# Optimization experiments

Measured on AMD Instinct MI355X. Metric: run time of the kernel, lower is better.

The kernel has to match this reference:

```python
import jax, jax.numpy as jnp
import numpy as np

N_NODES = 1_000_000   # total (cell x bin) pseudo nodes
FEAT_DIM = 128        # feature_dim
EMBED_DIM = 128       # embed_dim
BATCH = 8192          # nodes per forward batch
K = 10                # num_sample neighbors per node


def setup_inputs() -> dict:
    key = jax.random.key(0)
    k0, k1, k2, k3, k4 = jax.random.split(key, 5)
    emb = jax.random.normal(k0, (N_NODES, FEAT_DIM), dtype=jnp.float32)
    nodes = jax.random.randint(k1, (BATCH,), 0, N_NODES, dtype=jnp.int32)
    neigh_ids = jax.random.randint(k2, (BATCH, K), 0, N_NODES, dtype=jnp.int32)
    # strictly positive raw weights (contact counts); normalized per-row in forward
    neigh_w = jax.random.uniform(k3, (BATCH, K), dtype=jnp.float32, minval=1e-3, maxval=1.0)
    # nn.Linear(input_size * feat_dim, embed_dim), input_size = 2 (self + neighbors, gcn=False)
    W = jax.random.normal(k4, (2 * FEAT_DIM, EMBED_DIM), dtype=jnp.float32) / np.sqrt(2 * FEAT_DIM)
    b = jnp.zeros((EMBED_DIM,), dtype=jnp.float32)
    return {"emb": emb, "neigh_w": neigh_w, "W": W, "b": b,
            "nodes": nodes, "neigh_ids": neigh_ids}


def reference(emb, neigh_w, W, b, nodes, neigh_ids):
    # per-row weight normalization: w /= np.sum(w)  (weighted mean, replaces the COO spmm)
    w = neigh_w / jnp.sum(neigh_w, axis=1, keepdims=True)          # [B, K]
    neigh_feats = jnp.einsum('bk,bkd->bd', w, emb[neigh_ids])       # gather + weighted mean -> [B, D]
    self_feats = emb[nodes]                                         # [B, D]
    # gcn=False: concat self and aggregated neighbor features, then Linear + swish
    h = jnp.concatenate([self_feats, neigh_feats], axis=-1) @ W + b # [B, E]
    return h * jax.nn.sigmoid(h)                                    # swish activation
```

## Files before the change

kernel.cpp:

```cpp
#include <hip/hip_runtime.h>


#define B_NODES 8192
#define K_NEIGH 10
#define FDIM 128
#define EDIM 128
#define NPB 16
#define THREADS 256

typedef __attribute__((ext_vector_type(8))) short short8v;
typedef __attribute__((ext_vector_type(4))) float float4v;

__device__ __forceinline__ int swz(int byte) {
    return byte ^ (((byte >> 9) & 7) << 4);
}

__device__ __forceinline__ short f2bf(float f) {
    unsigned u = __builtin_bit_cast(unsigned, f);
    u += 0x7FFFu + ((u >> 16) & 1u);
    return (short)(u >> 16);
}

__global__ __launch_bounds__(THREADS, 2) void sage_fused(
    const float* __restrict__ emb,
    const float* __restrict__ neigh_w,
    const float* __restrict__ Wm,
    const float* __restrict__ bias,
    const int*   __restrict__ nodes,
    const int*   __restrict__ neigh_ids,
    float* __restrict__ out)
{
    __shared__ __align__(16) short x_lds[NPB * 2 * FDIM];
    char* xb = (char*)x_lds;

    const int tid = threadIdx.x;
    const int nb0 = blockIdx.x * NPB;

    {
        const int hw  = tid >> 5;
        const int l32 = tid & 31;
        const int d0  = l32 * 4;

        const int nA = hw * 2, nB = nA + 1;
        const int gA = nb0 + nA, gB = nb0 + nB;

        const int sidA = nodes[gA];
        const int sidB = nodes[gB];
        int idsA[K_NEIGH], idsB[K_NEIGH];
        float wA[K_NEIGH], wB[K_NEIGH];
#pragma unroll
        for (int k = 0; k < K_NEIGH; ++k) idsA[k] = neigh_ids[gA * K_NEIGH + k];
#pragma unroll
        for (int k = 0; k < K_NEIGH; ++k) idsB[k] = neigh_ids[gB * K_NEIGH + k];
        float wsA = 0.f, wsB = 0.f;
#pragma unroll
        for (int k = 0; k < K_NEIGH; ++k) { wA[k] = neigh_w[gA * K_NEIGH + k]; wsA += wA[k]; }
#pragma unroll
        for (int k = 0; k < K_NEIGH; ++k) { wB[k] = neigh_w[gB * K_NEIGH + k]; wsB += wB[k]; }
        const float invA = 1.f / wsA, invB = 1.f / wsB;

        {
            const float4 sv = *reinterpret_cast<const float4*>(&emb[(size_t)sidA * FDIM + d0]);
            float4 a = make_float4(0.f, 0.f, 0.f, 0.f);
#pragma unroll
            for (int k = 0; k < K_NEIGH; ++k) {
                const float4 v = *reinterpret_cast<const float4*>(&emb[(size_t)idsA[k] * FDIM + d0]);
                a.x = fmaf(wA[k], v.x, a.x); a.y = fmaf(wA[k], v.y, a.y);
                a.z = fmaf(wA[k], v.z, a.z); a.w = fmaf(wA[k], v.w, a.w);
            }
            ushort4 s4, g4;
            s4.x = (unsigned short)f2bf(sv.x); s4.y = (unsigned short)f2bf(sv.y);
            s4.z = (unsigned short)f2bf(sv.z); s4.w = (unsigned short)f2bf(sv.w);
            g4.x = (unsigned short)f2bf(a.x * invA); g4.y = (unsigned short)f2bf(a.y * invA);
            g4.z = (unsigned short)f2bf(a.z * invA); g4.w = (unsigned short)f2bf(a.w * invA);
            *reinterpret_cast<ushort4*>(xb + swz(nA * 512 + l32 * 8))       = s4;
            *reinterpret_cast<ushort4*>(xb + swz(nA * 512 + 256 + l32 * 8)) = g4;
        }
        {
            const float4 sv = *reinterpret_cast<const float4*>(&emb[(size_t)sidB * FDIM + d0]);
            float4 a = make_float4(0.f, 0.f, 0.f, 0.f);
#pragma unroll
            for (int k = 0; k < K_NEIGH; ++k) {
                const float4 v = *reinterpret_cast<const float4*>(&emb[(size_t)idsB[k] * FDIM + d0]);
                a.x = fmaf(wB[k], v.x, a.x); a.y = fmaf(wB[k], v.y, a.y);
                a.z = fmaf(wB[k], v.z, a.z); a.w = fmaf(wB[k], v.w, a.w);
            }
            ushort4 s4, g4;
            s4.x = (unsigned short)f2bf(sv.x); s4.y = (unsigned short)f2bf(sv.y);
            s4.z = (unsigned short)f2bf(sv.z); s4.w = (unsigned short)f2bf(sv.w);
            g4.x = (unsigned short)f2bf(a.x * invB); g4.y = (unsigned short)f2bf(a.y * invB);
            g4.z = (unsigned short)f2bf(a.z * invB); g4.w = (unsigned short)f2bf(a.w * invB);
            *reinterpret_cast<ushort4*>(xb + swz(nB * 512 + l32 * 8))       = s4;
            *reinterpret_cast<ushort4*>(xb + swz(nB * 512 + 256 + l32 * 8)) = g4;
        }
    }
    __syncthreads();

    {
        const int l    = tid & 63;
        const int wave = tid >> 6;
        const int lg   = l >> 4;
        const int li   = l & 15;

        float4v acc0 = {0.f, 0.f, 0.f, 0.f};
        float4v acc1 = {0.f, 0.f, 0.f, 0.f};
        const int e0 = wave * 32;

#pragma unroll
        for (int kblk = 0; kblk < 8; ++kblk) {
            const short8v a = *reinterpret_cast<const short8v*>(
                xb + swz(li * 512 + kblk * 64 + lg * 16));

            const int kb = kblk * 32 + lg * 8;
            short8v b0, b1;
#pragma unroll
            for (int j = 0; j < 8; ++j) {
                b0[j] = f2bf(Wm[(size_t)(kb + j) * EDIM + e0 + li]);
                b1[j] = f2bf(Wm[(size_t)(kb + j) * EDIM + e0 + 16 + li]);
            }
            acc0 = __builtin_amdgcn_mfma_f32_16x16x32_bf16(a, b0, acc0, 0, 0, 0);
            acc1 = __builtin_amdgcn_mfma_f32_16x16x32_bf16(a, b1, acc1, 0, 0, 0);
        }

        const float bv0 = bias[e0 + li];
        const float bv1 = bias[e0 + 16 + li];
#pragma unroll
        for (int r = 0; r < 4; ++r) {
            const int row = nb0 + lg * 4 + r;
            float v0 = acc0[r] + bv0;
            float v1 = acc1[r] + bv1;
            out[(size_t)row * EDIM + e0 + li]      = v0 / (1.f + __expf(-v0));
            out[(size_t)row * EDIM + e0 + 16 + li] = v1 / (1.f + __expf(-v1));
        }
    }
}

extern "C" void kernel_launch(void* const* d_in, const int* in_sizes, int n_in,
                              void* d_out, int out_size, void* d_ws, size_t ws_size,
                              hipStream_t stream) {
    const float* emb       = (const float*)d_in[0];
    const float* neigh_w   = (const float*)d_in[1];
    const float* Wm        = (const float*)d_in[2];
    const float* bias      = (const float*)d_in[3];
    const int*   nodes     = (const int*)d_in[4];
    const int*   neigh_ids = (const int*)d_in[5];
    float* out = (float*)d_out;

    sage_fused<<<dim3(B_NODES / NPB), dim3(THREADS), 0, stream>>>(
        emb, neigh_w, Wm, bias, nodes, neigh_ids, out);
}
```

Baseline: 16.40 us.

## Halve nodes per block and gather with full-wave float2 lanes per node

Cuts nodes per block from 16 to 8, doubling the grid to 1024 blocks, and raises the launch-bounds occupancy hint to 4. Each wave now gathers two nodes, with 64 lanes each loading float2 slices instead of 32 lanes loading float4. The neighbor id and weight loads are vectorized as int2/float2. The upper half of the LDS tile is zero-filled so the 16-row MFMA still runs, and only the 8 valid rows are written. The goal is more memory-level parallelism for the random embedding gathers, at the cost of wasting half of the MFMA work and reloading W per block twice as often overall.

```diff
diff --git a/kernel.cpp b/kernel.cpp
--- a/kernel.cpp
+++ b/kernel.cpp
@@ -5,7 +5,7 @@
 #define K_NEIGH 10
 #define FDIM 128
 #define EDIM 128
-#define NPB 16
+#define NPB 8
 #define THREADS 256
 
 typedef __attribute__((ext_vector_type(8))) short short8v;
@@ -21,7 +21,7 @@
     return (short)(u >> 16);
 }
 
-__global__ __launch_bounds__(THREADS, 2) void sage_fused(
+__global__ __launch_bounds__(THREADS, 4) void sage_fused(
     const float* __restrict__ emb,
     const float* __restrict__ neigh_w,
     const float* __restrict__ Wm,
@@ -30,81 +30,78 @@
     const int*   __restrict__ neigh_ids,
     float* __restrict__ out)
 {
-    __shared__ __align__(16) short x_lds[NPB * 2 * FDIM];
+    __shared__ __align__(16) short x_lds[16 * 2 * FDIM];
     char* xb = (char*)x_lds;
 
     const int tid = threadIdx.x;
     const int nb0 = blockIdx.x * NPB;
+    const int wv  = tid >> 6;
+    const int l   = tid & 63;
+
+    *reinterpret_cast<float4*>(xb + 4096 + tid * 16) = make_float4(0.f, 0.f, 0.f, 0.f);
 
     {
-        const int hw  = tid >> 5;
-        const int l32 = tid & 31;
-        const int d0  = l32 * 4;
+        const int d0 = l * 2;
+        const int nlA = wv * 2, nlB = nlA + 1;
+        const int gA = nb0 + nlA, gB = nb0 + nlB;
 
-        const int nA = hw * 2, nB = nA + 1;
-        const int gA = nb0 + nA, gB = nb0 + nB;
-
+        const int2*   ipA = reinterpret_cast<const int2*>(neigh_ids + (size_t)gA * K_NEIGH);
+        const int2*   ipB = reinterpret_cast<const int2*>(neigh_ids + (size_t)gB * K_NEIGH);
+        const float2* wpA = reinterpret_cast<const float2*>(neigh_w  + (size_t)gA * K_NEIGH);
+        const float2* wpB = reinterpret_cast<const float2*>(neigh_w  + (size_t)gB * K_NEIGH);
+        int2 idA[5], idB[5];
+        float2 wA[5], wB[5];
+#pragma unroll
+        for (int k = 0; k < 5; ++k) idA[k] = ipA[k];
+#pragma unroll
+        for (int k = 0; k < 5; ++k) idB[k] = ipB[k];
+#pragma unroll
+        for (int k = 0; k < 5; ++k) wA[k] = wpA[k];
+#pragma unroll
+        for (int k = 0; k < 5; ++k) wB[k] = wpB[k];
         const int sidA = nodes[gA];
         const int sidB = nodes[gB];
-        int idsA[K_NEIGH], idsB[K_NEIGH];
-        float wA[K_NEIGH], wB[K_NEIGH];
-#pragma unroll
-        for (int k = 0; k < K_NEIGH; ++k) idsA[k] = neigh_ids[gA * K_NEIGH + k];
-#pragma unroll
-        for (int k = 0; k < K_NEIGH; ++k) idsB[k] = neigh_ids[gB * K_NEIGH + k];
+
         float wsA = 0.f, wsB = 0.f;
 #pragma unroll
-        for (int k = 0; k < K_NEIGH; ++k) { wA[k] = neigh_w[gA * K_NEIGH + k]; wsA += wA[k]; }
-#pragma unroll
-        for (int k = 0; k < K_NEIGH; ++k) { wB[k] = neigh_w[gB * K_NEIGH + k]; wsB += wB[k]; }
+        for (int k = 0; k < 5; ++k) { wsA += wA[k].x + wA[k].y; wsB += wB[k].x + wB[k].y; }
         const float invA = 1.f / wsA, invB = 1.f / wsB;
 
-        {
-            const float4 sv = *reinterpret_cast<const float4*>(&emb[(size_t)sidA * FDIM + d0]);
-            float4 a = make_float4(0.f, 0.f, 0.f, 0.f);
+        const float2 svA = *reinterpret_cast<const float2*>(&emb[(size_t)sidA * FDIM + d0]);
+        const float2 svB = *reinterpret_cast<const float2*>(&emb[(size_t)sidB * FDIM + d0]);
+
+        float axA = 0.f, ayA = 0.f, axB = 0.f, ayB = 0.f;
 #pragma unroll
-            for (int k = 0; k < K_NEIGH; ++k) {
-                const float4 v = *reinterpret_cast<const float4*>(&emb[(size_t)idsA[k] * FDIM + d0]);
-                a.x = fmaf(wA[k], v.x, a.x); a.y = fmaf(wA[k], v.y, a.y);
-                a.z = fmaf(wA[k], v.z, a.z); a.w = fmaf(wA[k], v.w, a.w);
-            }
-            ushort4 s4, g4;
-            s4.x = (unsigned short)f2bf(sv.x); s4.y = (unsigned short)f2bf(sv.y);
-            s4.z = (unsigned short)f2bf(sv.z); s4.w = (unsigned short)f2bf(sv.w);
-            g4.x = (unsigned short)f2bf(a.x * invA); g4.y = (unsigned short)f2bf(a.y * invA);
-            g4.z = (unsigned short)f2bf(a.z * invA); g4.w = (unsigned short)f2bf(a.w * invA);
-            *reinterpret_cast<ushort4*>(xb + swz(nA * 512 + l32 * 8))       = s4;
-            *reinterpret_cast<ushort4*>(xb + swz(nA * 512 + 256 + l32 * 8)) = g4;
+        for (int k = 0; k < 5; ++k) {
+            const float2 vxA = *reinterpret_cast<const float2*>(&emb[(size_t)idA[k].x * FDIM + d0]);
+            const float2 vyA = *reinterpret_cast<const float2*>(&emb[(size_t)idA[k].y * FDIM + d0]);
+            const float2 vxB = *reinterpret_cast<const float2*>(&emb[(size_t)idB[k].x * FDIM + d0]);
+            const float2 vyB = *reinterpret_cast<const float2*>(&emb[(size_t)idB[k].y * FDIM + d0]);
+            axA = fmaf(wA[k].x, vxA.x, axA); ayA = fmaf(wA[k].x, vxA.y, ayA);
+            axA = fmaf(wA[k].y, vyA.x, axA); ayA = fmaf(wA[k].y, vyA.y, ayA);
+            axB = fmaf(wB[k].x, vxB.x, axB); ayB = fmaf(wB[k].x, vxB.y, ayB);
+            axB = fmaf(wB[k].y, vyB.x, axB); ayB = fmaf(wB[k].y, vyB.y, ayB);
         }
-        {
-            const float4 sv = *reinterpret_cast<const float4*>(&emb[(size_t)sidB * FDIM + d0]);
-            float4 a = make_float4(0.f, 0.f, 0.f, 0.f);
-#pragma unroll
-            for (int k = 0; k < K_NEIGH; ++k) {
-                const float4 v = *reinterpret_cast<const float4*>(&emb[(size_t)idsB[k] * FDIM + d0]);
-                a.x = fmaf(wB[k], v.x, a.x); a.y = fmaf(wB[k], v.y, a.y);
-                a.z = fmaf(wB[k], v.z, a.z); a.w = fmaf(wB[k], v.w, a.w);
-            }
-            ushort4 s4, g4;
-            s4.x = (unsigned short)f2bf(sv.x); s4.y = (unsigned short)f2bf(sv.y);
-            s4.z = (unsigned short)f2bf(sv.z); s4.w = (unsigned short)f2bf(sv.w);
-            g4.x = (unsigned short)f2bf(a.x * invB); g4.y = (unsigned short)f2bf(a.y * invB);
-            g4.z = (unsigned short)f2bf(a.z * invB); g4.w = (unsigned short)f2bf(a.w * invB);
-            *reinterpret_cast<ushort4*>(xb + swz(nB * 512 + l32 * 8))       = s4;
-            *reinterpret_cast<ushort4*>(xb + swz(nB * 512 + 256 + l32 * 8)) = g4;
-        }
+
+        ushort2 t;
+        t.x = (unsigned short)f2bf(svA.x); t.y = (unsigned short)f2bf(svA.y);
+        *reinterpret_cast<ushort2*>(xb + swz(nlA * 512 + l * 4)) = t;
+        t.x = (unsigned short)f2bf(axA * invA); t.y = (unsigned short)f2bf(ayA * invA);
+        *reinterpret_cast<ushort2*>(xb + swz(nlA * 512 + 256 + l * 4)) = t;
+        t.x = (unsigned short)f2bf(svB.x); t.y = (unsigned short)f2bf(svB.y);
+        *reinterpret_cast<ushort2*>(xb + swz(nlB * 512 + l * 4)) = t;
+        t.x = (unsigned short)f2bf(axB * invB); t.y = (unsigned short)f2bf(ayB * invB);
+        *reinterpret_cast<ushort2*>(xb + swz(nlB * 512 + 256 + l * 4)) = t;
     }
     __syncthreads();
 
     {
-        const int l    = tid & 63;
-        const int wave = tid >> 6;
-        const int lg   = l >> 4;
-        const int li   = l & 15;
+        const int lg = l >> 4;
+        const int li = l & 15;
+        const int e0 = wv * 32;
 
         float4v acc0 = {0.f, 0.f, 0.f, 0.f};
         float4v acc1 = {0.f, 0.f, 0.f, 0.f};
-        const int e0 = wave * 32;
 
 #pragma unroll
         for (int kblk = 0; kblk < 8; ++kblk) {
@@ -122,15 +119,17 @@
             acc1 = __builtin_amdgcn_mfma_f32_16x16x32_bf16(a, b1, acc1, 0, 0, 0);
         }
 
-        const float bv0 = bias[e0 + li];
-        const float bv1 = bias[e0 + 16 + li];
+        if (lg < 2) {
+            const float bv0 = bias[e0 + li];
+            const float bv1 = bias[e0 + 16 + li];
 #pragma unroll
-        for (int r = 0; r < 4; ++r) {
-            const int row = nb0 + lg * 4 + r;
-            float v0 = acc0[r] + bv0;
-            float v1 = acc1[r] + bv1;
-            out[(size_t)row * EDIM + e0 + li]      = v0 / (1.f + __expf(-v0));
-            out[(size_t)row * EDIM + e0 + 16 + li] = v1 / (1.f + __expf(-v1));
+            for (int r = 0; r < 4; ++r) {
+                const int row = nb0 + lg * 4 + r;
+                const float v0 = acc0[r] + bv0;
+                const float v1 = acc1[r] + bv1;
+                out[(size_t)row * EDIM + e0 + li]      = v0 / (1.f + __expf(-v0));
+                out[(size_t)row * EDIM + e0 + 16 + li] = v1 / (1.f + __expf(-v1));
+            }
         }
     }
 }
```

Measured after the change: 18.65 us. 1.14x slower.
